# Performance work log

Hardware: AMD Instinct MI355X
Metric: run time of the kernel (lower is better)

## Reference

```python
import jax, jax.numpy as jnp
import numpy as np

# H2RConfig constants
KERNEL = 3
MAX_ROUTES = 1000
STRIDE = 4.0
MIN_SIZE = 32.0
MAX_SIZE = 512.0
SCORE_POWER = 2.0
UNC_WEIGHT = 0.35


def setup_inputs() -> dict:
    key = jax.random.key(0)
    k1, k2, k3 = jax.random.split(key, 3)
    shape = (32, 1, 512, 512)  # [B, 1, H, W] heatmaps at stride 4
    return {
        "route_logits": jax.random.normal(k1, shape, jnp.float32),
        "scale_logits": jax.random.normal(k2, shape, jnp.float32),
        "uncertainty_logits": jax.random.normal(k3, shape, jnp.float32),
        "image_h": 2048,
        "image_w": 2048,
    }


def reference(route_logits, scale_logits, uncertainty_logits, image_h, image_w):
    # score map: sigmoid^power, modulated by uncertainty (use_route_uncertainty=True)
    score = jnp.power(jax.nn.sigmoid(route_logits), SCORE_POWER)
    score = score * (1.0 - UNC_WEIGHT * jax.nn.sigmoid(uncertainty_logits))

    # local-max NMS: 3x3 max pool, stride 1, SAME padding (torch pads with -inf)
    pooled = jax.lax.reduce_window(
        score, -jnp.inf, jax.lax.max,
        window_dimensions=(1, 1, KERNEL, KERNEL),
        window_strides=(1, 1, 1, 1),
        padding="SAME",
    )
    peak_mask = score == pooled
    filtered = jnp.where(peak_mask, score, -1.0)

    B = score.shape[0]
    Wd = score.shape[3]
    flat = filtered.reshape(B, -1)                 # [B, H*W]
    values, indices = jax.lax.top_k(flat, MAX_ROUTES)  # [B, K]
    valid = values > 0.0                            # torch drops these; we mask/pad

    ys = indices // Wd
    xs = indices % Wd
    cx = (xs.astype(jnp.float32) + 0.5) * STRIDE
    cy = (ys.astype(jnp.float32) + 0.5) * STRIDE

    # gather scale / uncertainty at peak locations
    sc = jnp.take_along_axis(scale_logits.reshape(B, -1), indices, axis=1)
    un = jax.nn.sigmoid(jnp.take_along_axis(uncertainty_logits.reshape(B, -1), indices, axis=1))

    side = MIN_SIZE + jax.nn.sigmoid(sc) * (MAX_SIZE - MIN_SIZE)
    side = side * (1.0 + 0.25 * un)
    half = side * 0.5

    iw = float(image_w)
    ih = float(image_h)
    x1 = jnp.clip(cx - half, 0.0, iw - 1.0)
    y1 = jnp.clip(cy - half, 0.0, ih - 1.0)
    x2 = jnp.clip(cx + half, 1.0, iw)
    y2 = jnp.clip(cy + half, 1.0, ih)

    bcol = jnp.broadcast_to(jnp.arange(B, dtype=jnp.float32)[:, None], values.shape)
    rois = jnp.stack([bcol, x1, y1, x2, y2], axis=-1)  # [B, K, 5]

    # padded (fixed-shape) equivalent of torch's variable-length concat
    rois = jnp.where(valid[..., None], rois, 0.0)
    scores = jnp.where(valid, values, 0.0)
    return rois, scores, valid
```

## Files before the change

kernel.cpp:

```cpp
#include <hip/hip_runtime.h>
#include <hip/hip_bf16.h>
#include <math.h>


#define B_   32
#define H_   512
#define W_   512
#define HW_  (H_ * W_)
#define K_   1000
#define ROWS_ 16
#define THR_  512
#define NSTRIP_ 32
#define SEGCAP_ 1200
#define NSLOT_ (NSTRIP_ * SEGCAP_)
#define NPAIR_ (NSLOT_ / 2)
#define CAND_ 2048
#define NBUK_ 4096
#define NW_   (NBUK_ / 2)

__device__ __forceinline__ float np_expf(float x) {
#pragma clang fp contract(off)
    const float log2e = 1.44269504088896341f;
    float z = x * log2e;
    float m = rintf(z);
    float r = fmaf(m, -0.693359375f, x);
    r = fmaf(m, 2.12194440e-4f, r);
    float r2 = r * r;
    float p = fmaf(1.9875691500e-4f, r, 1.3981999507e-3f);
    p = fmaf(p, r, 8.3334519073e-3f);
    p = fmaf(p, r, 4.1665795894e-2f);
    p = fmaf(p, r, 1.6666665459e-1f);
    p = fmaf(p, r, 5.0000001201e-1f);
    p = fmaf(p, r2, r);
    p = p + 1.0f;
    int mi = (int)m;
    float sc = __int_as_float((127 + mi) << 23);
    return p * sc;
}

__device__ __forceinline__ float sigmoid_np(float x) {
#pragma clang fp contract(off)
    float e = np_expf(-x);
    float d = 1.0f + e;
    return 1.0f / d;
}

__device__ __forceinline__ float score_ref(float r, float u) {
#pragma clang fp contract(off)
    float s  = sigmoid_np(r);
    float s2 = s * s;
    float su = sigmoid_np(u);
    float t  = 0.35f * su;
    float m  = 1.0f - t;
    return s2 * m;
}

__device__ __forceinline__ float sigmoid_fast(float x) {
    return 1.0f / (1.0f + __expf(-x));
}

__global__ __launch_bounds__(THR_, 4) void fused_peak_kernel(
    const float* __restrict__ route, const float* __restrict__ unc,
    unsigned long long* __restrict__ plist)
{
    __shared__ float sm[ROWS_ + 2][W_];
    __shared__ int lcnt;

    const int tid   = threadIdx.x;
    const int lane  = tid & 63;
    const int strip = blockIdx.x;
    const int b     = blockIdx.y;
    const int r0    = strip * ROWS_;
    if (tid == 0) lcnt = 0;

    const float4* rb4 = (const float4*)(route + (size_t)b * HW_);
    const float4* ub4 = (const float4*)(unc   + (size_t)b * HW_);
    unsigned long long* seg =
        plist + (size_t)(b * NSTRIP_ + strip) * SEGCAP_;

    float4 rv[5], uv[5];
    int lrow[5], c4[5]; bool ok[5];
    #pragma unroll
    for (int k = 0; k < 5; ++k) {
        int slot = tid + k * THR_;
        slot = slot < 2303 ? slot : 2303;
        int row = slot >> 7;
        int gy  = r0 - 1 + row;
        lrow[k] = row; c4[k] = slot & 127;
        ok[k]   = (gy >= 0 && gy < H_);
        int cy  = gy < 0 ? 0 : (gy >= H_ ? H_ - 1 : gy);
        rv[k] = rb4[cy * 128 + c4[k]];
        uv[k] = ub4[cy * 128 + c4[k]];
    }
    #pragma unroll
    for (int k = 0; k < 5; ++k) {
        float4 s;
        s.x = score_ref(rv[k].x, uv[k].x);
        s.y = score_ref(rv[k].y, uv[k].y);
        s.z = score_ref(rv[k].z, uv[k].z);
        s.w = score_ref(rv[k].w, uv[k].w);
        if (!ok[k]) { s.x = -INFINITY; s.y = -INFINITY;
                      s.z = -INFINITY; s.w = -INFINITY; }
        *(float4*)&sm[lrow[k]][c4[k] * 4] = s;
    }
    __syncthreads();

    #pragma unroll
    for (int j = 0; j < 4; ++j) {
        int g  = tid + j * THR_;
        int ly = 1 + (g >> 7);
        int x0 = (g & 127) * 4;
        int gy = r0 + (ly - 1);
        float4 q0 = *(const float4*)&sm[ly - 1][x0];
        float4 q1 = *(const float4*)&sm[ly    ][x0];
        float4 q2 = *(const float4*)&sm[ly + 1][x0];
        bool hasL = (x0 > 0), hasR = (x0 + 4 < W_);
        float l0 = hasL ? sm[ly - 1][x0 - 1] : -INFINITY;
        float l1 = hasL ? sm[ly    ][x0 - 1] : -INFINITY;
        float l2 = hasL ? sm[ly + 1][x0 - 1] : -INFINITY;
        float e0 = hasR ? sm[ly - 1][x0 + 4] : -INFINITY;
        float e1 = hasR ? sm[ly    ][x0 + 4] : -INFINITY;
        float e2 = hasR ? sm[ly + 1][x0 + 4] : -INFINITY;
        float f_m1 = fmaxf(l0, fmaxf(l1, l2));
        float f_0  = fmaxf(q0.x, fmaxf(q1.x, q2.x));
        float f_1  = fmaxf(q0.y, fmaxf(q1.y, q2.y));
        float f_2  = fmaxf(q0.z, fmaxf(q1.z, q2.z));
        float f_3  = fmaxf(q0.w, fmaxf(q1.w, q2.w));
        float f_4  = fmaxf(e0, fmaxf(e1, e2));
        float tb0  = fmaxf(q0.x, q2.x);
        float tb1  = fmaxf(q0.y, q2.y);
        float tb2  = fmaxf(q0.z, q2.z);
        float tb3  = fmaxf(q0.w, q2.w);
        float vv[4] = { q1.x, q1.y, q1.z, q1.w };
        float mm[4];
        mm[0] = fmaxf(fmaxf(f_m1, f_1), tb0);
        mm[1] = fmaxf(fmaxf(f_0,  f_2), tb1);
        mm[2] = fmaxf(fmaxf(f_1,  f_3), tb2);
        mm[3] = fmaxf(fmaxf(f_2,  f_4), tb3);
        #pragma unroll
        for (int i = 0; i < 4; ++i) {
            bool take = (vv[i] >= mm[i]);
            unsigned long long mk = __ballot(take);
            if (mk) {
                int ldr = __ffsll((unsigned long long)mk) - 1;
                int base_ = 0;
                if (lane == ldr) base_ = atomicAdd(&lcnt, __popcll(mk));
                base_ = __shfl(base_, ldr, 64);
                if (take) {
                    int p = base_ + __popcll(mk & ((1ull << lane) - 1ull));
                    unsigned int bits = __float_as_uint(vv[i]);
                    unsigned int idx  = (unsigned int)(gy * W_ + x0 + i);
                    if (p < SEGCAP_)
                        seg[p] = ((unsigned long long)bits << 32)
                                 | (0xFFFFFFFFu - idx);
                }
            }
        }
    }
    __syncthreads();
    int n = lcnt < SEGCAP_ ? lcnt : SEGCAP_;
    for (int i = n + tid; i < SEGCAP_; i += THR_) seg[i] = 0ull;
}

__global__ __launch_bounds__(1024) void select_kernel(
    const float* __restrict__ scale, const float* __restrict__ unc,
    const unsigned long long* __restrict__ plist,
    const int* __restrict__ ih_p, const int* __restrict__ iw_p,
    float* __restrict__ out)
{
    __shared__ unsigned int h4[4 * NW_];
    __shared__ unsigned long long cand[CAND_];
    __shared__ int sh_T, sh_n;

    const int b = blockIdx.x, tid = threadIdx.x;
    const int lane = tid & 63, wid = tid >> 6;
    if (tid == 0) { sh_T = 0; sh_n = 0; }
    for (int i = tid; i < 4 * NW_; i += 1024) h4[i] = 0u;
    __syncthreads();

    const ulonglong2* p2 =
        (const ulonglong2*)(plist + (size_t)b * NSLOT_);
    unsigned int* hw = h4 + (wid >> 2) * NW_;

    {
        int i = tid;
        for (; i + 1024 < NPAIR_; i += 2048) {
            ulonglong2 a = p2[i];
            ulonglong2 c = p2[i + 1024];
            unsigned int b0 = ((unsigned int)(a.x >> 32)) >> 18;
            unsigned int b1 = ((unsigned int)(a.y >> 32)) >> 18;
            unsigned int b2 = ((unsigned int)(c.x >> 32)) >> 18;
            unsigned int b3 = ((unsigned int)(c.y >> 32)) >> 18;
            if (b0) atomicAdd(&hw[b0 >> 1], 1u << ((b0 & 1) * 16));
            if (b1) atomicAdd(&hw[b1 >> 1], 1u << ((b1 & 1) * 16));
            if (b2) atomicAdd(&hw[b2 >> 1], 1u << ((b2 & 1) * 16));
            if (b3) atomicAdd(&hw[b3 >> 1], 1u << ((b3 & 1) * 16));
        }
        for (; i < NPAIR_; i += 1024) {
            ulonglong2 a = p2[i];
            unsigned int b0 = ((unsigned int)(a.x >> 32)) >> 18;
            unsigned int b1 = ((unsigned int)(a.y >> 32)) >> 18;
            if (b0) atomicAdd(&hw[b0 >> 1], 1u << ((b0 & 1) * 16));
            if (b1) atomicAdd(&hw[b1 >> 1], 1u << ((b1 & 1) * 16));
        }
    }
    __syncthreads();
    for (int i = tid; i < NW_; i += 1024)
        h4[i] = h4[i] + h4[NW_ + i] + h4[2 * NW_ + i] + h4[3 * NW_ + i];
    __syncthreads();

    if (wid == 0) {
        int total = 0;
        for (int c = NBUK_ / 64 - 1; c >= 0; --c) {
            int bucket = c * 64 + lane;
            int cnt = (int)((h4[bucket >> 1] >> ((bucket & 1) * 16)) & 0xFFFFu);
            int sum = cnt;
            #pragma unroll
            for (int off = 32; off > 0; off >>= 1)
                sum += __shfl_down(sum, off, 64);
            sum = __shfl(sum, 0, 64);
            if (total + sum < K_) { total += sum; continue; }
            int suf = cnt;
            #pragma unroll
            for (int off = 1; off < 64; off <<= 1) {
                int o = __shfl_down(suf, off, 64);
                suf += (lane + off < 64) ? o : 0;
            }
            bool cond = (total + suf) >= K_;
            unsigned long long mask = __ballot(cond);
            int ls = 63 - __builtin_clzll(mask);
            if (lane == 0) sh_T = c * 64 + ls;
            break;
        }
    }
    __syncthreads();
    const unsigned int T = (unsigned int)sh_T;

    {
        int i = tid;
        for (; i + 1024 < NPAIR_; i += 2048) {
            ulonglong2 a = p2[i];
            ulonglong2 c = p2[i + 1024];
            unsigned long long ks[4] = { a.x, a.y, c.x, c.y };
            #pragma unroll
            for (int q = 0; q < 4; ++q) {
                bool take = ((((unsigned int)(ks[q] >> 32))) >> 18) >= T;
                unsigned long long mk = __ballot(take);
                if (mk) {
                    int ldr = __ffsll((unsigned long long)mk) - 1;
                    int base_ = 0;
                    if (lane == ldr) base_ = atomicAdd(&sh_n, __popcll(mk));
                    base_ = __shfl(base_, ldr, 64);
                    if (take) {
                        int p = base_ + __popcll(mk & ((1ull << lane) - 1ull));
                        if (p < CAND_) cand[p] = ks[q];
                    }
                }
            }
        }
        for (; i < NPAIR_; i += 1024) {
            ulonglong2 a = p2[i];
            unsigned long long ks[2] = { a.x, a.y };
            #pragma unroll
            for (int q = 0; q < 2; ++q) {
                bool take = ((((unsigned int)(ks[q] >> 32))) >> 18) >= T;
                unsigned long long mk = __ballot(take);
                if (mk) {
                    int ldr = __ffsll((unsigned long long)mk) - 1;
                    int base_ = 0;
                    if (lane == ldr) base_ = atomicAdd(&sh_n, __popcll(mk));
                    base_ = __shfl(base_, ldr, 64);
                    if (take) {
                        int p = base_ + __popcll(mk & ((1ull << lane) - 1ull));
                        if (p < CAND_) cand[p] = ks[q];
                    }
                }
            }
        }
    }
    __syncthreads();
    int nc = sh_n; if (nc > CAND_) nc = CAND_;
    int sortN = (nc <= 1024) ? 1024 : CAND_;
    for (int i = tid; i < sortN; i += 1024)
        if (i >= nc) cand[i] = 0ull;

    for (int kk = 2; kk <= sortN; kk <<= 1) {
        for (int jj = kk >> 1; jj > 0; jj >>= 1) {
            __syncthreads();
            for (int p = tid; p < (sortN >> 1); p += 1024) {
                int i   = ((p & ~(jj - 1)) << 1) | (p & (jj - 1));
                int ixj = i | jj;
                bool desc = ((i & kk) == 0);
                unsigned long long a = cand[i], c2 = cand[ixj];
                if (desc ? (a < c2) : (a > c2)) { cand[i] = c2; cand[ixj] = a; }
            }
        }
    }
    __syncthreads();

    const float fih = (float)(*ih_p);
    const float fiw = (float)(*iw_p);
    float* rois   = out;
    float* scores = out + (size_t)B_ * K_ * 5;
    float* validf = out + (size_t)B_ * K_ * 6;

    for (int k = tid; k < K_; k += 1024) {
        int o = b * K_ + k;
        unsigned long long key = cand[k];
        unsigned int bits = (unsigned int)(key >> 32);
        if (bits == 0u) {
            rois[o * 5 + 0] = 0.0f; rois[o * 5 + 1] = 0.0f;
            rois[o * 5 + 2] = 0.0f; rois[o * 5 + 3] = 0.0f;
            rois[o * 5 + 4] = 0.0f;
            scores[o] = 0.0f; validf[o] = 0.0f;
        } else {
            float v = __uint_as_float(bits);
            unsigned int idx = 0xFFFFFFFFu - (unsigned int)(key & 0xFFFFFFFFull);
            int y = (int)(idx >> 9), x = (int)(idx & 511u);
            float cx = ((float)x + 0.5f) * 4.0f;
            float cy = ((float)y + 0.5f) * 4.0f;
            float ss = sigmoid_fast(scale[(size_t)b * HW_ + idx]);
            float su = sigmoid_fast(unc  [(size_t)b * HW_ + idx]);
            float side = (32.0f + ss * 480.0f) * (1.0f + 0.25f * su);
            float half = 0.5f * side;
            float x1 = fminf(fmaxf(cx - half, 0.0f), fiw - 1.0f);
            float y1 = fminf(fmaxf(cy - half, 0.0f), fih - 1.0f);
            float x2 = fminf(fmaxf(cx + half, 1.0f), fiw);
            float y2 = fminf(fmaxf(cy + half, 1.0f), fih);
            rois[o * 5 + 0] = (float)b;
            rois[o * 5 + 1] = x1; rois[o * 5 + 2] = y1;
            rois[o * 5 + 3] = x2; rois[o * 5 + 4] = y2;
            scores[o] = v; validf[o] = 1.0f;
        }
    }
}

extern "C" void kernel_launch(void* const* d_in, const int* in_sizes, int n_in,
                              void* d_out, int out_size, void* d_ws, size_t ws_size,
                              hipStream_t stream) {
    const float* route = (const float*)d_in[0];
    const float* scale = (const float*)d_in[1];
    const float* unc   = (const float*)d_in[2];
    const int*   ih    = (const int*)d_in[3];
    const int*   iw    = (const int*)d_in[4];
    float* out = (float*)d_out;

    unsigned long long* plist = (unsigned long long*)d_ws;

    dim3 g(NSTRIP_, B_);
    fused_peak_kernel<<<g, THR_, 0, stream>>>(route, unc, plist);
    select_kernel<<<B_, 1024, 0, stream>>>(scale, unc, plist, ih, iw, out);
}
```

Before: 163.8 us.

## Build histogram in peak kernel and split candidate gather across blocks

Moves the score-bucket histogram into the peak-detection kernel, where per-strip shared histograms are merged into a global per-batch histogram with atomics. The old single-block-per-batch select kernel is split in two: a gather kernel that uses 8 blocks per batch to pick candidates above the threshold via global atomics, and a sort/emit kernel. This targets the serial plist pass in select, which ran on only 32 blocks, by spreading that work across more of the GPU. The cost is an extra memset, an extra launch, global atomics, and a candidate order that is no longer deterministic before sorting.

Measured after the change: 271.2 us. +65.6%, slower.

```diff
diff --git a/kernel.cpp b/kernel.cpp
--- a/kernel.cpp
+++ b/kernel.cpp
@@ -16,7 +16,10 @@
 #define NPAIR_ (NSLOT_ / 2)
 #define CAND_ 2048
 #define NBUK_ 4096
-#define NW_   (NBUK_ / 2)
+#define GSPLIT_ 8
+
+#define PL_BYTES_ ((size_t)B_ * NSLOT_ * 8)
+#define GH_BYTES_ ((size_t)B_ * NBUK_ * 4)
 
 __device__ __forceinline__ float np_expf(float x) {
 #pragma clang fp contract(off)
@@ -61,7 +64,8 @@
 
 __global__ __launch_bounds__(THR_, 4) void fused_peak_kernel(
     const float* __restrict__ route, const float* __restrict__ unc,
-    unsigned long long* __restrict__ plist)
+    unsigned long long* __restrict__ plist,
+    unsigned int* __restrict__ ghist)
 {
     __shared__ float sm[ROWS_ + 2][W_];
     __shared__ int lcnt;
@@ -105,6 +109,7 @@
     }
     __syncthreads();
 
+    unsigned int hreg[8];
     #pragma unroll
     for (int j = 0; j < 4; ++j) {
         int g  = tid + j * THR_;
@@ -137,6 +142,7 @@
         mm[1] = fmaxf(fmaxf(f_0,  f_2), tb1);
         mm[2] = fmaxf(fmaxf(f_1,  f_3), tb2);
         mm[3] = fmaxf(fmaxf(f_2,  f_4), tb3);
+        unsigned int pk01 = 0u, pk23 = 0u;
         #pragma unroll
         for (int i = 0; i < 4; ++i) {
             bool take = (vv[i] >= mm[i]);
@@ -150,70 +156,74 @@
                     int p = base_ + __popcll(mk & ((1ull << lane) - 1ull));
                     unsigned int bits = __float_as_uint(vv[i]);
                     unsigned int idx  = (unsigned int)(gy * W_ + x0 + i);
-                    if (p < SEGCAP_)
+                    if (p < SEGCAP_) {
                         seg[p] = ((unsigned long long)bits << 32)
                                  | (0xFFFFFFFFu - idx);
+                        unsigned int bkt = bits >> 18;
+                        if (i < 2) pk01 |= bkt << (16 * i);
+                        else       pk23 |= bkt << (16 * (i - 2));
+                    }
                 }
             }
         }
-    }
-    __syncthreads();
+        hreg[2 * j]     = pk01;
+        hreg[2 * j + 1] = pk23;
+    }
+    __syncthreads();
+
+    unsigned int* hist = (unsigned int*)&sm[0][0];
+    for (int i = tid; i < NBUK_; i += THR_) hist[i] = 0u;
     int n = lcnt < SEGCAP_ ? lcnt : SEGCAP_;
     for (int i = n + tid; i < SEGCAP_; i += THR_) seg[i] = 0ull;
-}
-
-__global__ __launch_bounds__(1024) void select_kernel(
-    const float* __restrict__ scale, const float* __restrict__ unc,
+    __syncthreads();
+
+    #pragma unroll
+    for (int j = 0; j < 8; ++j) {
+        unsigned int h  = hreg[j];
+        unsigned int b0 = h & 0xFFFFu;
+        unsigned int b1 = h >> 16;
+        if (b0) atomicAdd(&hist[b0], 1u);
+        if (b1) atomicAdd(&hist[b1], 1u);
+    }
+    __syncthreads();
+
+    unsigned int* gh = ghist + (size_t)b * NBUK_;
+    for (int i = tid; i < NBUK_; i += THR_) {
+        unsigned int c = hist[i];
+        if (c) atomicAdd(&gh[i], c);
+    }
+}
+
+__global__ __launch_bounds__(1024) void gather_kernel(
     const unsigned long long* __restrict__ plist,
-    const int* __restrict__ ih_p, const int* __restrict__ iw_p,
-    float* __restrict__ out)
+    const unsigned int* __restrict__ ghist,
+    int* __restrict__ gcnt,
+    unsigned long long* __restrict__ gcand)
 {
-    __shared__ unsigned int h4[4 * NW_];
-    __shared__ unsigned long long cand[CAND_];
-    __shared__ int sh_T, sh_n;
-
-    const int b = blockIdx.x, tid = threadIdx.x;
+    __shared__ int sh_T;
+
+    const int sp  = blockIdx.x;
+    const int b   = blockIdx.y;
+    const int tid = threadIdx.x;
     const int lane = tid & 63, wid = tid >> 6;
-    if (tid == 0) { sh_T = 0; sh_n = 0; }
-    for (int i = tid; i < 4 * NW_; i += 1024) h4[i] = 0u;
-    __syncthreads();
-
-    const ulonglong2* p2 =
-        (const ulonglong2*)(plist + (size_t)b * NSLOT_);
-    unsigned int* hw = h4 + (wid >> 2) * NW_;
-
+
+    const ulonglong2* p2 = (const ulonglong2*)(plist + (size_t)b * NSLOT_);
+    const int i0 = sp * (NPAIR_ / GSPLIT_);
+    const int i1 = i0 + (NPAIR_ / GSPLIT_);
+
+    ulonglong2 a[3]; int ni = 0;
     {
-        int i = tid;
-        for (; i + 1024 < NPAIR_; i += 2048) {
-            ulonglong2 a = p2[i];
-            ulonglong2 c = p2[i + 1024];
-            unsigned int b0 = ((unsigned int)(a.x >> 32)) >> 18;
-            unsigned int b1 = ((unsigned int)(a.y >> 32)) >> 18;
-            unsigned int b2 = ((unsigned int)(c.x >> 32)) >> 18;
-            unsigned int b3 = ((unsigned int)(c.y >> 32)) >> 18;
-            if (b0) atomicAdd(&hw[b0 >> 1], 1u << ((b0 & 1) * 16));
-            if (b1) atomicAdd(&hw[b1 >> 1], 1u << ((b1 & 1) * 16));
-            if (b2) atomicAdd(&hw[b2 >> 1], 1u << ((b2 & 1) * 16));
-            if (b3) atomicAdd(&hw[b3 >> 1], 1u << ((b3 & 1) * 16));
-        }
-        for (; i < NPAIR_; i += 1024) {
-            ulonglong2 a = p2[i];
-            unsigned int b0 = ((unsigned int)(a.x >> 32)) >> 18;
-            unsigned int b1 = ((unsigned int)(a.y >> 32)) >> 18;
-            if (b0) atomicAdd(&hw[b0 >> 1], 1u << ((b0 & 1) * 16));
-            if (b1) atomicAdd(&hw[b1 >> 1], 1u << ((b1 & 1) * 16));
-        }
-    }
-    __syncthreads();
-    for (int i = tid; i < NW_; i += 1024)
-        h4[i] = h4[i] + h4[NW_ + i] + h4[2 * NW_ + i] + h4[3 * NW_ + i];
-    __syncthreads();
-
+        int k = 0;
+        for (int i = i0 + tid; i < i1; i += 1024, ++k) a[k] = p2[i];
+        ni = k;
+    }
+
+    if (tid == 0) sh_T = 0;
     if (wid == 0) {
+        const unsigned int* gh = ghist + (size_t)b * NBUK_;
         int total = 0;
         for (int c = NBUK_ / 64 - 1; c >= 0; --c) {
-            int bucket = c * 64 + lane;
-            int cnt = (int)((h4[bucket >> 1] >> ((bucket & 1) * 16)) & 0xFFFFu);
+            int cnt = (int)gh[c * 64 + lane];
             int sum = cnt;
             #pragma unroll
             for (int off = 32; off > 0; off >>= 1)
@@ -234,55 +244,46 @@
         }
     }
     __syncthreads();
-    const unsigned int T = (unsigned int)sh_T;
-
-    {
-        int i = tid;
-        for (; i + 1024 < NPAIR_; i += 2048) {
-            ulonglong2 a = p2[i];
-            ulonglong2 c = p2[i + 1024];
-            unsigned long long ks[4] = { a.x, a.y, c.x, c.y };
-            #pragma unroll
-            for (int q = 0; q < 4; ++q) {
-                bool take = ((((unsigned int)(ks[q] >> 32))) >> 18) >= T;
-                unsigned long long mk = __ballot(take);
-                if (mk) {
-                    int ldr = __ffsll((unsigned long long)mk) - 1;
-                    int base_ = 0;
-                    if (lane == ldr) base_ = atomicAdd(&sh_n, __popcll(mk));
-                    base_ = __shfl(base_, ldr, 64);
-                    if (take) {
-                        int p = base_ + __popcll(mk & ((1ull << lane) - 1ull));
-                        if (p < CAND_) cand[p] = ks[q];
-                    }
+    unsigned int T = (unsigned int)sh_T;
+    if (T == 0u) T = 1u;
+
+    int* cnt = gcnt + b;
+    unsigned long long* cd = gcand + (size_t)b * CAND_;
+    for (int k = 0; k < ni; ++k) {
+        unsigned long long ks[2] = { a[k].x, a[k].y };
+        #pragma unroll
+        for (int q = 0; q < 2; ++q) {
+            bool take = ((((unsigned int)(ks[q] >> 32))) >> 18) >= T;
+            unsigned long long mk = __ballot(take);
+            if (mk) {
+                int ldr = __ffsll((unsigned long long)mk) - 1;
+                int base_ = 0;
+                if (lane == ldr) base_ = atomicAdd(cnt, __popcll(mk));
+                base_ = __shfl(base_, ldr, 64);
+                if (take) {
+                    int p = base_ + __popcll(mk & ((1ull << lane) - 1ull));
+                    if (p < CAND_) cd[p] = ks[q];
                 }
             }
         }
-        for (; i < NPAIR_; i += 1024) {
-            ulonglong2 a = p2[i];
-            unsigned long long ks[2] = { a.x, a.y };
-            #pragma unroll
-            for (int q = 0; q < 2; ++q) {
-                bool take = ((((unsigned int)(ks[q] >> 32))) >> 18) >= T;
-                unsigned long long mk = __ballot(take);
-                if (mk) {
-                    int ldr = __ffsll((unsigned long long)mk) - 1;
-                    int base_ = 0;
-                    if (lane == ldr) base_ = atomicAdd(&sh_n, __popcll(mk));
-                    base_ = __shfl(base_, ldr, 64);
-                    if (take) {
-                        int p = base_ + __popcll(mk & ((1ull << lane) - 1ull));
-                        if (p < CAND_) cand[p] = ks[q];
-                    }
-                }
-            }
-        }
-    }
-    __syncthreads();
-    int nc = sh_n; if (nc > CAND_) nc = CAND_;
+    }
+}
+
+__global__ __launch_bounds__(1024) void sort_emit_kernel(
+    const float* __restrict__ scale, const float* __restrict__ unc,
+    const unsigned long long* __restrict__ gcand,
+    const int* __restrict__ gcnt,
+    const int* __restrict__ ih_p, const int* __restrict__ iw_p,
+    float* __restrict__ out)
+{
+    __shared__ unsigned long long cand[CAND_];
+
+    const int b = blockIdx.x, tid = threadIdx.x;
+    int nc = gcnt[b]; if (nc > CAND_) nc = CAND_;
     int sortN = (nc <= 1024) ? 1024 : CAND_;
+    const unsigned long long* cd = gcand + (size_t)b * CAND_;
     for (int i = tid; i < sortN; i += 1024)
-        if (i >= nc) cand[i] = 0ull;
+        cand[i] = (i < nc) ? cd[i] : 0ull;
 
     for (int kk = 2; kk <= sortN; kk <<= 1) {
         for (int jj = kk >> 1; jj > 0; jj >>= 1) {
@@ -345,9 +346,19 @@
     const int*   iw    = (const int*)d_in[4];
     float* out = (float*)d_out;
 
-    unsigned long long* plist = (unsigned long long*)d_ws;
+    unsigned char* base = (unsigned char*)d_ws;
+    unsigned long long* plist = (unsigned long long*)base;
+    unsigned int* ghist = (unsigned int*)(base + PL_BYTES_);
+    int* gcnt           = (int*)(base + PL_BYTES_ + GH_BYTES_);
+    unsigned long long* gcand =
+        (unsigned long long*)(base + PL_BYTES_ + GH_BYTES_ + 128);
+
+    hipMemsetAsync(ghist, 0, GH_BYTES_ + 128, stream);
 
     dim3 g(NSTRIP_, B_);
-    fused_peak_kernel<<<g, THR_, 0, stream>>>(route, unc, plist);
-    select_kernel<<<B_, 1024, 0, stream>>>(scale, unc, plist, ih, iw, out);
-}
+    fused_peak_kernel<<<g, THR_, 0, stream>>>(route, unc, plist, ghist);
+    dim3 gg(GSPLIT_, B_);
+    gather_kernel<<<gg, 1024, 0, stream>>>(plist, ghist, gcnt, gcand);
+    sort_emit_kernel<<<B_, 1024, 0, stream>>>(scale, unc, gcand, gcnt,
+                                              ih, iw, out);
+}
```
